# Kernel tuning notes

Hardware: AMD Instinct MI355X
Metric: run time of the kernel (lower is better)

## Reference

```python
import jax, jax.numpy as jnp
import numpy as np

B, C, H, E, K, QT = 256, 1024, 64, 64, 2, 20000

def _mlp(x, W1, b1, W2, b2):
    # GKT MLP (eval mode: dropout off; batch-norm omitted, see notes)
    return jax.nn.relu(jax.nn.relu(x @ W1 + b1) @ W2 + b2)

def setup_inputs() -> dict:
    key = jax.random.key(0)
    ks = jax.random.split(key, 30)
    s = 0.05  # weight scale to keep pre-clamp activations in a sane range
    xt = jax.random.uniform(ks[0], (B,), dtype=jnp.float32)
    qt = jax.random.randint(ks[1], (B,), 0, QT)
    ht = jax.random.normal(ks[2], (B, C, H), dtype=jnp.float32)
    # binary question->concept incidence, ~4 KCs per question, col 0 forced on
    oh = (jax.random.uniform(ks[3], (QT, C)) < 4.0 / C).astype(jnp.float32)
    oh = oh.at[:, 0].set(1.0)
    qt_kc_one_hot = jnp.concatenate([oh, jnp.zeros((1, C), jnp.float32)], axis=0)  # zero padding row
    kc_embeddings = jax.random.normal(ks[4], (C, E), dtype=jnp.float32) * 0.1
    graphs = jax.random.uniform(ks[5], (K, C, C), dtype=jnp.float32)  # graph_model output
    neigh_weight = jnp.float32(0.8)
    MI = H + E
    Ws1 = jax.random.normal(ks[6], (MI, H), jnp.float32) * s; bs1 = jnp.zeros((H,), jnp.float32)
    Ws2 = jax.random.normal(ks[7], (H, H), jnp.float32) * s;  bs2 = jnp.zeros((H,), jnp.float32)
    Wn1 = jax.random.normal(ks[8], (K, 2 * MI, H), jnp.float32) * s; bn1 = jnp.zeros((K, H), jnp.float32)
    Wn2 = jax.random.normal(ks[9], (K, H, H), jnp.float32) * s;      bn2 = jnp.zeros((K, H), jnp.float32)
    ea_w = jax.random.uniform(ks[10], (C,), dtype=jnp.float32)
    We = jax.random.normal(ks[11], (H, H), jnp.float32) * s; be = jnp.zeros((H,), jnp.float32)
    Wa = jax.random.normal(ks[12], (H, H), jnp.float32) * s; ba = jnp.zeros((H,), jnp.float32)
    W_ih = jax.random.normal(ks[13], (H, 3 * H), jnp.float32) * s; b_ih = jnp.zeros((3 * H,), jnp.float32)
    W_hh = jax.random.normal(ks[14], (H, 3 * H), jnp.float32) * s; b_hh = jnp.zeros((3 * H,), jnp.float32)
    Wp = jax.random.normal(ks[15], (H, 1), jnp.float32) * s; bp = jnp.zeros((1,), jnp.float32)
    return dict(xt=xt, qt=qt, ht=ht, qt_kc_one_hot=qt_kc_one_hot, kc_embeddings=kc_embeddings,
                graphs=graphs, neigh_weight=neigh_weight, Ws1=Ws1, bs1=bs1, Ws2=Ws2, bs2=bs2,
                Wn1=Wn1, bn1=bn1, Wn2=Wn2, bn2=bn2, ea_w=ea_w, We=We, be=be, Wa=Wa, ba=ba,
                W_ih=W_ih, b_ih=b_ih, W_hh=W_hh, b_hh=b_hh, Wp=Wp, bp=bp)

def reference(xt, qt, ht, qt_kc_one_hot, kc_embeddings, graphs, neigh_weight,
              Ws1, bs1, Ws2, bs2, Wn1, bn1, Wn2, bn2, ea_w, We, be, Wa, ba,
              W_ih, b_ih, W_hh, b_hh, Wp, bp):
    # ---- _aggregate: the fusion loops never write back, so tmp_ht = cat(ht, kc_emb)
    mask = qt_kc_one_hot[qt]                                   # [B, C] gather of binary incidence
    kc = jnp.broadcast_to(kc_embeddings[None], (mask.shape[0], C, E))
    tmp_ht = jnp.concatenate([ht, kc], axis=-1)                # [B, C, H+E]
    # ---- _agg_neighbors
    self_ht = tmp_ht * mask[..., None]
    self_feat = jnp.clip(_mlp(self_ht, Ws1, bs1, Ws2, bs2), -10.0, 10.0)
    neigh_ht = jnp.clip(jnp.concatenate([self_ht, tmp_ht], axis=-1), -5.0, 5.0)  # [B,C,2(H+E)]
    # bug-faithful adj: mean of graphs[k] rows over sample 0's active concepts
    a0 = mask[0]                                               # [C]
    denom = jnp.maximum(a0.sum(), 1.0)
    adj = jnp.clip(jnp.einsum('c,kcd->kd', a0, graphs) / denom, -5.0, 5.0)       # [K, C]
    nb = jax.vmap(lambda W1, b1, W2, b2: _mlp(neigh_ht, W1, b1, W2, b2))(Wn1, bn1, Wn2, bn2)
    nb = jnp.clip(nb, -5.0, 5.0)                               # [K, B, C, H]
    w = jnp.clip(neigh_weight, 0.1, 0.9)
    nf = jnp.clip(adj[0][None, :, None] * nb[0], -5.0, 5.0)
    for k in range(1, K):
        nf = jnp.clip(w * nf + (1.0 - w) * adj[k][None, :, None] * nb[k], -5.0, 5.0)
    m_next = jnp.clip(jnp.where(mask[..., None] > 0.5, self_feat, nf), -50.0, 50.0)
    # ---- erase-add gate
    g = ea_w[None, :, None]
    res = m_next - g * jax.nn.sigmoid(m_next @ We + be) * m_next + g * jnp.tanh(m_next @ Wa + ba)
    # ---- GRUCell over flattened (B*C) rows
    gi = res @ W_ih + b_ih
    gh = ht @ W_hh + b_hh
    ir, iz, in_ = jnp.split(gi, 3, axis=-1)
    hr, hz, hn = jnp.split(gh, 3, axis=-1)
    r = jax.nn.sigmoid(ir + hr)
    z = jax.nn.sigmoid(iz + hz)
    n = jnp.tanh(in_ + r * hn)
    h_next = (1.0 - z) * n + z * ht                            # [B, C, H]
    y = jax.nn.sigmoid(h_next @ Wp + bp)[..., 0]               # [B, C]
    return y
```

## Files before the change

### kernel.cpp

```cpp
#include <hip/hip_runtime.h>

#define DEVINL __device__ __forceinline__

typedef __bf16 bf16x8 __attribute__((ext_vector_type(8)));
typedef float  f32x4  __attribute__((ext_vector_type(4)));

static constexpr size_t kAdjOff  = 0;
static constexpr size_t kBiasOff = 8192;
static constexpr size_t kFragOff = 8192 + 786432;

static constexpr int FB_Wn1h0 = 0,  FB_Wn1h1 = 8,  FB_Wn2_0 = 16, FB_Wn2_1 = 24;
static constexpr int FB_Ws1h  = 32, FB_Ws2   = 40, FB_We    = 48, FB_Wa    = 56;
static constexpr int FB_Wih   = 64, FB_Whh   = 88;

DEVINL unsigned short bf16r(float f) {
  unsigned u = __builtin_bit_cast(unsigned, f);
  unsigned r = ((u >> 16) & 1u) + 0x7FFFu;
  return (unsigned short)((u + r) >> 16);
}
DEVINL float sigmoidf_(float x) { return __builtin_amdgcn_rcpf(1.f + __expf(-x)); }
DEVINL float tanhf_(float x)    { return 1.f - 2.f * __builtin_amdgcn_rcpf(1.f + __expf(2.f * x)); }

DEVINL void lds_fence() {
  __builtin_amdgcn_sched_barrier(0);
  __builtin_amdgcn_s_waitcnt(0xC07F);
  __builtin_amdgcn_sched_barrier(0);
}

DEVINL f32x4 mfma16(bf16x8 a, bf16x8 b, f32x4 c) {
  return __builtin_amdgcn_mfma_f32_16x16x32_bf16(a, b, c, 0, 0, 0);
}

DEVINL unsigned clip2_(unsigned x) {
  float lo = __builtin_bit_cast(float, x << 16);
  float hi = __builtin_bit_cast(float, x & 0xFFFF0000u);
  lo = fminf(fmaxf(lo, -5.f), 5.f);
  hi = fminf(fmaxf(hi, -5.f), 5.f);
  return (__builtin_bit_cast(unsigned, lo) >> 16) | (__builtin_bit_cast(unsigned, hi) & 0xFFFF0000u);
}
DEVINL bf16x8 clip5(bf16x8 a) {
  uint4 u = __builtin_bit_cast(uint4, a);
  u.x = clip2_(u.x); u.y = clip2_(u.y); u.z = clip2_(u.z); u.w = clip2_(u.w);
  return __builtin_bit_cast(bf16x8, u);
}

__global__ void prep_adj_kernel(const int* __restrict__ qt, const float* __restrict__ onehot,
                                const float* __restrict__ graphs, float* __restrict__ adjw) {
  __shared__ float a0v[1024];
  __shared__ int   aidx[1024];
  __shared__ int   s_nnz;
  __shared__ float s_den;
  const int tid = threadIdx.x;
  const int k = blockIdx.x >> 2, chunk = blockIdx.x & 3;
  if (tid == 0) { s_nnz = 0; s_den = 0.f; }
  __syncthreads();
  const int q0 = qt[0];
  float lsum = 0.f;
#pragma unroll
  for (int i = 0; i < 4; i++) {
    int c = tid * 4 + i;
    float v = onehot[(size_t)q0 * 1024 + c];
    lsum += v;
    if (v != 0.f) { int p = atomicAdd(&s_nnz, 1); aidx[p] = c; a0v[p] = v; }
  }
#pragma unroll
  for (int off = 32; off >= 1; off >>= 1) lsum += __shfl_xor(lsum, off, 64);
  if ((tid & 63) == 0) atomicAdd(&s_den, lsum);
  __syncthreads();
  const float denom = fmaxf(s_den, 1.f);
  const int nnz = s_nnz;
  const int d = chunk * 256 + tid;
  const float* G = graphs + (size_t)k * 1048576 + d;
  float sum = 0.f;
  for (int j = 0; j < nnz; j++) sum += a0v[j] * G[(size_t)aidx[j] * 1024];
  adjw[k * 1024 + d] = fminf(fmaxf(sum / denom, -5.f), 5.f);
}

__global__ void prep_bias_kernel(const float* __restrict__ kc, const float* __restrict__ Wn1,
                                 const float* __restrict__ bn1, const float* __restrict__ Ws1,
                                 const float* __restrict__ bs1, float* __restrict__ biasTab) {
  int gid = blockIdx.x * 256 + threadIdx.x;
  int j = gid & 63;
  int c = (gid >> 6) & 1023;
  int tab = gid >> 16;
  const float* kcr = kc + (size_t)c * 64;
  float s;
  if (tab < 2) {
    s = bn1[tab * 64 + j];
    const float* W = Wn1 + ((size_t)tab * 256 + 192) * 64 + j;
#pragma unroll 4
    for (int e = 0; e < 64; e++) s += fminf(fmaxf(kcr[e], -5.f), 5.f) * W[(size_t)e * 64];
  } else {
    s = bs1[j];
    const float* W = Ws1 + (size_t)64 * 64 + j;
#pragma unroll 4
    for (int e = 0; e < 64; e++) s += kcr[e] * W[(size_t)e * 64];
  }
  int c16 = c >> 4, rr = c & 3, qq = (c & 15) >> 2, nt = j >> 4;
  int lane = qq * 16 + (j & 15);
  biasTab[(size_t)((((c16 * 3 + tab) * 4 + nt) * 64 + lane)) * 4 + rr] = s;
}

__global__ void prep_wfrag_kernel(const float* __restrict__ Wn1, const float* __restrict__ Wn2,
                                  const float* __restrict__ Ws1, const float* __restrict__ Ws2,
                                  const float* __restrict__ We,  const float* __restrict__ Wa,
                                  const float* __restrict__ Wih, const float* __restrict__ Whh,
                                  uint4* __restrict__ wfrag) {
  const int bid = blockIdx.x, lane = threadIdx.x;
  int mat, ks, nt;
  if (bid < 64) { mat = bid >> 3; ks = (bid >> 2) & 1; nt = bid & 3; }
  else { int f2 = bid - 64; mat = 8 + f2 / 24; int f = f2 % 24; ks = f / 12; nt = f % 12; }
  const float* base = Wn1; int stride = 64;
  switch (mat) {
    case 0: base = Wn1 + (size_t)128 * 64; break;
    case 1: base = Wn1 + (size_t)(256 + 128) * 64; break;
    case 2: base = Wn2; break;
    case 3: base = Wn2 + (size_t)64 * 64; break;
    case 4: base = Ws1; break;
    case 5: base = Ws2; break;
    case 6: base = We; break;
    case 7: base = Wa; break;
    case 8: base = Wih; stride = 192; break;
    case 9: base = Whh; stride = 192; break;
  }
  const int qq = lane >> 4, col = nt * 16 + (lane & 15);
  union { unsigned short u[8]; uint4 v; } tmp;
#pragma unroll
  for (int jj = 0; jj < 8; jj++) {
    int k = ks * 32 + qq * 8 + jj;
    tmp.u[jj] = bf16r(base[(size_t)k * stride + col]);
  }
  wfrag[(size_t)bid * 64 + lane] = tmp.v;
}

__global__ __launch_bounds__(256, 2) void gkt_main_kernel(
    const int* __restrict__ qt, const float* __restrict__ onehot, const float* __restrict__ ht,
    const float* __restrict__ nw, const float* __restrict__ bn2, const float* __restrict__ be,
    const float* __restrict__ ba, const float* __restrict__ bih, const float* __restrict__ bhh,
    const float* __restrict__ Wp, const float* __restrict__ bp, const float* __restrict__ eaw,
    const float* __restrict__ bs2, const float* __restrict__ adjw, const float* __restrict__ biasTab,
    const bf16x8* __restrict__ wfrag, float* __restrict__ out) {
  __shared__ __align__(16) unsigned short hbuf[4][32][72];
  __shared__ __align__(16) float tokp[4][128];

  const int tid = threadIdx.x;
  const int wv = tid >> 6, lane = tid & 63;
  const int q = lane >> 4, cl = lane & 15;
  const int t0 = (blockIdx.x * 4 + wv) * 32;
  const int b = t0 >> 10, c0 = t0 & 1023, c16 = c0 >> 4;

  unsigned short* hb = &hbuf[wv][0][0];
  float* tp = &tokp[wv][0];

  if (lane < 32) {
    const int c = c0 + lane;
    tp[lane]      = onehot[(size_t)qt[b] * 1024 + c];
    tp[32 + lane] = adjw[c];
    tp[64 + lane] = adjw[1024 + c];
    tp[96 + lane] = eaw[c];
  }
  {
    const float4* ht4 = (const float4*)ht;
#pragma unroll
    for (int i = 0; i < 8; i++) {
      float4 v = ht4[(size_t)t0 * 16 + i * 64 + lane];
      int e = i * 64 + lane;
      int tok = e >> 4, coll = (e & 15) * 4;
      ushort4 h;
      h.x = bf16r(v.x); h.y = bf16r(v.y); h.z = bf16r(v.z); h.w = bf16r(v.w);
      *(ushort4*)&hbuf[wv][tok][coll] = h;
    }
  }
  lds_fence();

  const float wmix = fminf(fmaxf(nw[0], 0.1f), 0.9f);
  float wp4[4];
#pragma unroll
  for (int nt = 0; nt < 4; nt++) wp4[nt] = Wp[nt * 16 + cl];
  const float bpv = bp[0];

  auto ldA = [&](int mt, int ks) -> bf16x8 {
    return *(const bf16x8*)(hb + (cl + 16 * mt) * 72 + ks * 32 + q * 8);
  };
  auto ldB = [&](int frag) -> bf16x8 { return wfrag[frag * 64 + lane]; };
  auto ldTP4 = [&](int base, int mt) -> f32x4 {
    return *(const f32x4*)(tp + base + 16 * mt + q * 4);
  };
  const f32x4* bt4 = (const f32x4*)biasTab;

  bf16x8 xr[2][2];
#pragma unroll
  for (int mt = 0; mt < 2; mt++)
#pragma unroll
    for (int ks = 0; ks < 2; ks++) xr[mt][ks] = ldA(mt, ks);
  lds_fence();

  f32x4 nf[2][4];
  {
    bf16x8 xc[2][2];
#pragma unroll
    for (int mt = 0; mt < 2; mt++)
#pragma unroll
      for (int ks = 0; ks < 2; ks++) xc[mt][ks] = clip5(xr[mt][ks]);

#pragma unroll
    for (int k2 = 0; k2 < 2; k2++) {
      f32x4 acc[2][4];
#pragma unroll
      for (int mt = 0; mt < 2; mt++)
#pragma unroll
        for (int nt = 0; nt < 4; nt++)
          acc[mt][nt] = bt4[(((c16 + mt) * 3 + k2) * 4 + nt) * 64 + lane];
#pragma unroll
      for (int ks = 0; ks < 2; ks++)
#pragma unroll
        for (int nt = 0; nt < 4; nt++) {
          bf16x8 bb = ldB((k2 ? FB_Wn1h1 : FB_Wn1h0) + ks * 4 + nt);
          acc[0][nt] = mfma16(xc[0][ks], bb, acc[0][nt]);
          acc[1][nt] = mfma16(xc[1][ks], bb, acc[1][nt]);
        }
#pragma unroll
      for (int mt = 0; mt < 2; mt++)
#pragma unroll
        for (int nt = 0; nt < 4; nt++)
#pragma unroll
          for (int r = 0; r < 4; r++)
            hb[(16 * mt + q * 4 + r) * 72 + nt * 16 + cl] = bf16r(fmaxf(acc[mt][nt][r], 0.f));
      lds_fence();
      f32x4 acc2[2][4];
#pragma unroll
      for (int nt = 0; nt < 4; nt++) {
        float bz = bn2[k2 * 64 + nt * 16 + cl];
        f32x4 iv = {bz, bz, bz, bz};
        acc2[0][nt] = iv; acc2[1][nt] = iv;
      }
#pragma unroll
      for (int ks = 0; ks < 2; ks++) {
        bf16x8 a0 = ldA(0, ks), a1 = ldA(1, ks);
#pragma unroll
        for (int nt = 0; nt < 4; nt++) {
          bf16x8 bb = ldB((k2 ? FB_Wn2_1 : FB_Wn2_0) + ks * 4 + nt);
          acc2[0][nt] = mfma16(a0, bb, acc2[0][nt]);
          acc2[1][nt] = mfma16(a1, bb, acc2[1][nt]);
        }
      }
      lds_fence();
#pragma unroll
      for (int mt = 0; mt < 2; mt++) {
        f32x4 adjv = ldTP4((1 + k2) * 32, mt);
#pragma unroll
        for (int nt = 0; nt < 4; nt++)
#pragma unroll
          for (int r = 0; r < 4; r++) {
            float nb = fminf(fmaxf(acc2[mt][nt][r], 0.f), 5.f);
            float v = adjv[r] * nb;
            if (k2 == 0) nf[mt][nt][r] = wmix * fminf(fmaxf(v, -5.f), 5.f);
            else         nf[mt][nt][r] = fminf(fmaxf(nf[mt][nt][r] + (1.f - wmix) * v, -5.f), 5.f);
          }
      }
    }
  }

  bool anySelf = __any((lane < 32) && (tp[lane] > 0.5f));
  if (anySelf) {
    f32x4 acc[2][4];
#pragma unroll
    for (int mt = 0; mt < 2; mt++)
#pragma unroll
      for (int nt = 0; nt < 4; nt++)
        acc[mt][nt] = bt4[(((c16 + mt) * 3 + 2) * 4 + nt) * 64 + lane];
#pragma unroll
    for (int ks = 0; ks < 2; ks++)
#pragma unroll
      for (int nt = 0; nt < 4; nt++) {
        bf16x8 bb = ldB(FB_Ws1h + ks * 4 + nt);
        acc[0][nt] = mfma16(xr[0][ks], bb, acc[0][nt]);
        acc[1][nt] = mfma16(xr[1][ks], bb, acc[1][nt]);
      }
#pragma unroll
    for (int mt = 0; mt < 2; mt++)
#pragma unroll
      for (int nt = 0; nt < 4; nt++)
#pragma unroll
        for (int r = 0; r < 4; r++)
          hb[(16 * mt + q * 4 + r) * 72 + nt * 16 + cl] = bf16r(fmaxf(acc[mt][nt][r], 0.f));
    lds_fence();
    f32x4 acc2[2][4];
#pragma unroll
    for (int nt = 0; nt < 4; nt++) {
      float bz = bs2[nt * 16 + cl];
      f32x4 iv = {bz, bz, bz, bz};
      acc2[0][nt] = iv; acc2[1][nt] = iv;
    }
#pragma unroll
    for (int ks = 0; ks < 2; ks++) {
      bf16x8 a0 = ldA(0, ks), a1 = ldA(1, ks);
#pragma unroll
      for (int nt = 0; nt < 4; nt++) {
        bf16x8 bb = ldB(FB_Ws2 + ks * 4 + nt);
        acc2[0][nt] = mfma16(a0, bb, acc2[0][nt]);
        acc2[1][nt] = mfma16(a1, bb, acc2[1][nt]);
      }
    }
    lds_fence();
#pragma unroll
    for (int mt = 0; mt < 2; mt++) {
      f32x4 mk = ldTP4(0, mt);
#pragma unroll
      for (int nt = 0; nt < 4; nt++)
#pragma unroll
        for (int r = 0; r < 4; r++) {
          float sf = fminf(fmaxf(acc2[mt][nt][r], 0.f), 10.f);
          nf[mt][nt][r] = (mk[r] > 0.5f) ? sf : nf[mt][nt][r];
        }
    }
  }

#pragma unroll
  for (int mt = 0; mt < 2; mt++)
#pragma unroll
    for (int nt = 0; nt < 4; nt++)
#pragma unroll
      for (int r = 0; r < 4; r++)
        hb[(16 * mt + q * 4 + r) * 72 + nt * 16 + cl] = bf16r(nf[mt][nt][r]);
  lds_fence();
#pragma unroll
  for (int mt = 0; mt < 2; mt++) {
    bf16x8 mf0 = ldA(mt, 0), mf1 = ldA(mt, 1);
    f32x4 gv = ldTP4(96, mt);
    {
      f32x4 accE[4];
#pragma unroll
      for (int nt = 0; nt < 4; nt++) {
        float bz = be[nt * 16 + cl];
        accE[nt] = {bz, bz, bz, bz};
      }
#pragma unroll
      for (int nt = 0; nt < 4; nt++) {
        accE[nt] = mfma16(mf0, ldB(FB_We + nt), accE[nt]);
        accE[nt] = mfma16(mf1, ldB(FB_We + 4 + nt), accE[nt]);
      }
#pragma unroll
      for (int nt = 0; nt < 4; nt++)
#pragma unroll
        for (int r = 0; r < 4; r++) {
          float m = nf[mt][nt][r];
          nf[mt][nt][r] = m - gv[r] * sigmoidf_(accE[nt][r]) * m;
        }
    }
    {
      f32x4 accA[4];
#pragma unroll
      for (int nt = 0; nt < 4; nt++) {
        float bz = ba[nt * 16 + cl];
        accA[nt] = {bz, bz, bz, bz};
      }
#pragma unroll
      for (int nt = 0; nt < 4; nt++) {
        accA[nt] = mfma16(mf0, ldB(FB_Wa + nt), accA[nt]);
        accA[nt] = mfma16(mf1, ldB(FB_Wa + 4 + nt), accA[nt]);
      }
#pragma unroll
      for (int nt = 0; nt < 4; nt++)
#pragma unroll
        for (int r = 0; r < 4; r++)
          nf[mt][nt][r] += gv[r] * tanhf_(accA[nt][r]);
    }
  }

  lds_fence();
#pragma unroll
  for (int mt = 0; mt < 2; mt++)
#pragma unroll
    for (int nt = 0; nt < 4; nt++)
#pragma unroll
      for (int r = 0; r < 4; r++)
        hb[(16 * mt + q * 4 + r) * 72 + nt * 16 + cl] = bf16r(nf[mt][nt][r]);
  lds_fence();

#pragma unroll
  for (int mt = 0; mt < 2; mt++) {
    bf16x8 rf0 = ldA(mt, 0), rf1 = ldA(mt, 1);
    f32x4 gR[4], gZ[4], gN[4], gH[4];
#pragma unroll
    for (int nt = 0; nt < 4; nt++) {
      int col = nt * 16 + cl;
      float brz = bih[col] + bhh[col];
      float bzz = bih[64 + col] + bhh[64 + col];
      float bnn = bih[128 + col];
      float bhn = bhh[128 + col];
      gR[nt] = {brz, brz, brz, brz};
      gZ[nt] = {bzz, bzz, bzz, bzz};
      gN[nt] = {bnn, bnn, bnn, bnn};
      gH[nt] = {bhn, bhn, bhn, bhn};
    }
#pragma unroll
    for (int ks = 0; ks < 2; ks++) {
      bf16x8 rfk = ks ? rf1 : rf0;
      bf16x8 xrk = xr[mt][ks];
#pragma unroll
      for (int nt = 0; nt < 4; nt++) {
        gR[nt] = mfma16(rfk, ldB(FB_Wih + ks * 12 + nt), gR[nt]);
        gR[nt] = mfma16(xrk, ldB(FB_Whh + ks * 12 + nt), gR[nt]);
        gZ[nt] = mfma16(rfk, ldB(FB_Wih + ks * 12 + 4 + nt), gZ[nt]);
        gZ[nt] = mfma16(xrk, ldB(FB_Whh + ks * 12 + 4 + nt), gZ[nt]);
        gN[nt] = mfma16(rfk, ldB(FB_Wih + ks * 12 + 8 + nt), gN[nt]);
        gH[nt] = mfma16(xrk, ldB(FB_Whh + ks * 12 + 8 + nt), gH[nt]);
      }
    }
#pragma unroll
    for (int r = 0; r < 4; r++) {
      int tok = 16 * mt + q * 4 + r;
      float part = 0.f;
#pragma unroll
      for (int nt = 0; nt < 4; nt++) {
        float rr = sigmoidf_(gR[nt][r]);
        float zz = sigmoidf_(gZ[nt][r]);
        float nval = tanhf_(gN[nt][r] + rr * gH[nt][r]);
        float htv = ht[(size_t)(t0 + tok) * 64 + nt * 16 + cl];
        float hnx = (1.f - zz) * nval + zz * htv;
        part += hnx * wp4[nt];
      }
      part += __shfl_xor(part, 1, 64);
      part += __shfl_xor(part, 2, 64);
      part += __shfl_xor(part, 4, 64);
      part += __shfl_xor(part, 8, 64);
      if (cl == 0) out[t0 + tok] = sigmoidf_(part + bpv);
    }
  }
}

extern "C" void kernel_launch(void* const* d_in, const int* in_sizes, int n_in,
                              void* d_out, int out_size, void* d_ws, size_t ws_size,
                              hipStream_t stream) {
  const int*   qt     = (const int*)d_in[1];
  const float* ht     = (const float*)d_in[2];
  const float* onehot = (const float*)d_in[3];
  const float* kc     = (const float*)d_in[4];
  const float* graphs = (const float*)d_in[5];
  const float* nw     = (const float*)d_in[6];
  const float* Ws1    = (const float*)d_in[7];
  const float* bs1    = (const float*)d_in[8];
  const float* Ws2    = (const float*)d_in[9];
  const float* bs2    = (const float*)d_in[10];
  const float* Wn1    = (const float*)d_in[11];
  const float* bn1    = (const float*)d_in[12];
  const float* Wn2    = (const float*)d_in[13];
  const float* bn2    = (const float*)d_in[14];
  const float* eaw    = (const float*)d_in[15];
  const float* We     = (const float*)d_in[16];
  const float* be     = (const float*)d_in[17];
  const float* Wa     = (const float*)d_in[18];
  const float* ba     = (const float*)d_in[19];
  const float* Wih    = (const float*)d_in[20];
  const float* bih    = (const float*)d_in[21];
  const float* Whh    = (const float*)d_in[22];
  const float* bhh    = (const float*)d_in[23];
  const float* Wp     = (const float*)d_in[24];
  const float* bp     = (const float*)d_in[25];
  float* out = (float*)d_out;

  float* adjw    = (float*)((char*)d_ws + kAdjOff);
  float* biasTab = (float*)((char*)d_ws + kBiasOff);
  uint4* wfragU  = (uint4*)((char*)d_ws + kFragOff);

  prep_adj_kernel<<<8, 256, 0, stream>>>(qt, onehot, graphs, adjw);
  prep_bias_kernel<<<768, 256, 0, stream>>>(kc, Wn1, bn1, Ws1, bs1, biasTab);
  prep_wfrag_kernel<<<112, 64, 0, stream>>>(Wn1, Wn2, Ws1, Ws2, We, Wa, Wih, Whh, wfragU);
  gkt_main_kernel<<<2048, 256, 0, stream>>>(qt, onehot, ht, nw, bn2, be, ba, bih, bhh,
                                            Wp, bp, eaw, bs2, adjw, biasTab,
                                            (const bf16x8*)wfragU, out);
}
```

Baseline: 275.9 us.

## Transpose MFMA operands so accumulators hold token-major rows, vectorize LDS stores

Swaps the MFMA operand order so weights are the A operand and activations the B operand. Each lane's accumulator then holds 4 consecutive feature columns of one token, so bf16 results can be packed and written to LDS as 8-byte stores instead of scalar 2-byte stores. Biases, ht and Wp become float4 loads, the final dot-product reduction needs only two cross-lane shuffles, and the bias table layout is rearranged to match. The LDS scratch is widened to 136 columns so both Wn1 hidden halves and the pre- and post-gate activations live side by side, which removes some fences at the cost of more shared memory per block.

```diff
diff --git a/kernel.cpp b/kernel.cpp
--- a/kernel.cpp
+++ b/kernel.cpp
@@ -18,6 +18,13 @@
   unsigned r = ((u >> 16) & 1u) + 0x7FFFu;
   return (unsigned short)((u + r) >> 16);
 }
+DEVINL unsigned pack2(float a, float b) {
+  unsigned ua = __builtin_bit_cast(unsigned, a);
+  unsigned ub = __builtin_bit_cast(unsigned, b);
+  ua += ((ua >> 16) & 1u) + 0x7FFFu;
+  ub += ((ub >> 16) & 1u) + 0x7FFFu;
+  return (ua >> 16) | (ub & 0xFFFF0000u);
+}
 DEVINL float sigmoidf_(float x) { return __builtin_amdgcn_rcpf(1.f + __expf(-x)); }
 DEVINL float tanhf_(float x)    { return 1.f - 2.f * __builtin_amdgcn_rcpf(1.f + __expf(2.f * x)); }
 
@@ -27,8 +34,8 @@
   __builtin_amdgcn_sched_barrier(0);
 }
 
-DEVINL f32x4 mfma16(bf16x8 a, bf16x8 b, f32x4 c) {
-  return __builtin_amdgcn_mfma_f32_16x16x32_bf16(a, b, c, 0, 0, 0);
+DEVINL f32x4 mfmaWX(bf16x8 w, bf16x8 x, f32x4 c) {
+  return __builtin_amdgcn_mfma_f32_16x16x32_bf16(w, x, c, 0, 0, 0);
 }
 
 DEVINL unsigned clip2_(unsigned x) {
@@ -96,9 +103,8 @@
 #pragma unroll 4
     for (int e = 0; e < 64; e++) s += kcr[e] * W[(size_t)e * 64];
   }
-  int c16 = c >> 4, rr = c & 3, qq = (c & 15) >> 2, nt = j >> 4;
-  int lane = qq * 16 + (j & 15);
-  biasTab[(size_t)((((c16 * 3 + tab) * 4 + nt) * 64 + lane)) * 4 + rr] = s;
+  int c16p = c >> 4, cl2 = c & 15, nt = j >> 4, qq = (j >> 2) & 3, rr = j & 3;
+  biasTab[((size_t)(((c16p * 3 + tab) * 16 + cl2) * 4 + nt) * 4 + qq) * 4 + rr] = s;
 }
 
 __global__ void prep_wfrag_kernel(const float* __restrict__ Wn1, const float* __restrict__ Wn2,
@@ -140,7 +146,7 @@
     const float* __restrict__ Wp, const float* __restrict__ bp, const float* __restrict__ eaw,
     const float* __restrict__ bs2, const float* __restrict__ adjw, const float* __restrict__ biasTab,
     const bf16x8* __restrict__ wfrag, float* __restrict__ out) {
-  __shared__ __align__(16) unsigned short hbuf[4][32][72];
+  __shared__ __align__(16) unsigned short sbuf[4][32][136];
   __shared__ __align__(16) float tokp[4][128];
 
   const int tid = threadIdx.x;
@@ -149,7 +155,7 @@
   const int t0 = (blockIdx.x * 4 + wv) * 32;
   const int b = t0 >> 10, c0 = t0 & 1023, c16 = c0 >> 4;
 
-  unsigned short* hb = &hbuf[wv][0][0];
+  unsigned short* sb = &sbuf[wv][0][0];
   float* tp = &tokp[wv][0];
 
   if (lane < 32) {
@@ -166,33 +172,33 @@
       float4 v = ht4[(size_t)t0 * 16 + i * 64 + lane];
       int e = i * 64 + lane;
       int tok = e >> 4, coll = (e & 15) * 4;
-      ushort4 h;
-      h.x = bf16r(v.x); h.y = bf16r(v.y); h.z = bf16r(v.z); h.w = bf16r(v.w);
-      *(ushort4*)&hbuf[wv][tok][coll] = h;
+      uint2 p = {pack2(v.x, v.y), pack2(v.z, v.w)};
+      *(uint2*)&sbuf[wv][tok][coll] = p;
     }
   }
   lds_fence();
 
   const float wmix = fminf(fmaxf(nw[0], 0.1f), 0.9f);
-  float wp4[4];
-#pragma unroll
-  for (int nt = 0; nt < 4; nt++) wp4[nt] = Wp[nt * 16 + cl];
   const float bpv = bp[0];
 
-  auto ldA = [&](int mt, int ks) -> bf16x8 {
-    return *(const bf16x8*)(hb + (cl + 16 * mt) * 72 + ks * 32 + q * 8);
+  auto ldS = [&](int mt, int base) -> bf16x8 {
+    return *(const bf16x8*)(sb + (cl + 16 * mt) * 136 + base + q * 8);
   };
   auto ldB = [&](int frag) -> bf16x8 { return wfrag[frag * 64 + lane]; };
-  auto ldTP4 = [&](int base, int mt) -> f32x4 {
-    return *(const f32x4*)(tp + base + 16 * mt + q * 4);
+  auto stW = [&](int mt, int colb, f32x4 v) {
+    uint2 p = {pack2(v[0], v[1]), pack2(v[2], v[3])};
+    *(uint2*)(sb + (cl + 16 * mt) * 136 + colb) = p;
   };
   const f32x4* bt4 = (const f32x4*)biasTab;
+  auto ldBias = [&](int mt, int tab, int nt) -> f32x4 {
+    return bt4[(((c16 + mt) * 3 + tab) * 16 + cl) * 16 + nt * 4 + q];
+  };
 
   bf16x8 xr[2][2];
 #pragma unroll
   for (int mt = 0; mt < 2; mt++)
 #pragma unroll
-    for (int ks = 0; ks < 2; ks++) xr[mt][ks] = ldA(mt, ks);
+    for (int ks = 0; ks < 2; ks++) xr[mt][ks] = ldS(mt, ks * 32);
   lds_fence();
 
   f32x4 nf[2][4];
@@ -209,56 +215,60 @@
 #pragma unroll
       for (int mt = 0; mt < 2; mt++)
 #pragma unroll
-        for (int nt = 0; nt < 4; nt++)
-          acc[mt][nt] = bt4[(((c16 + mt) * 3 + k2) * 4 + nt) * 64 + lane];
+        for (int nt = 0; nt < 4; nt++) acc[mt][nt] = ldBias(mt, k2, nt);
 #pragma unroll
       for (int ks = 0; ks < 2; ks++)
 #pragma unroll
         for (int nt = 0; nt < 4; nt++) {
           bf16x8 bb = ldB((k2 ? FB_Wn1h1 : FB_Wn1h0) + ks * 4 + nt);
-          acc[0][nt] = mfma16(xc[0][ks], bb, acc[0][nt]);
-          acc[1][nt] = mfma16(xc[1][ks], bb, acc[1][nt]);
+          acc[0][nt] = mfmaWX(bb, xc[0][ks], acc[0][nt]);
+          acc[1][nt] = mfmaWX(bb, xc[1][ks], acc[1][nt]);
         }
 #pragma unroll
       for (int mt = 0; mt < 2; mt++)
 #pragma unroll
-        for (int nt = 0; nt < 4; nt++)
-#pragma unroll
-          for (int r = 0; r < 4; r++)
-            hb[(16 * mt + q * 4 + r) * 72 + nt * 16 + cl] = bf16r(fmaxf(acc[mt][nt][r], 0.f));
-      lds_fence();
+        for (int nt = 0; nt < 4; nt++) {
+          f32x4 rv;
+#pragma unroll
+          for (int r = 0; r < 4; r++) rv[r] = fmaxf(acc[mt][nt][r], 0.f);
+          stW(mt, k2 * 64 + nt * 16 + q * 4, rv);
+        }
+    }
+    lds_fence();
+
+#pragma unroll
+    for (int k2 = 0; k2 < 2; k2++) {
       f32x4 acc2[2][4];
 #pragma unroll
       for (int nt = 0; nt < 4; nt++) {
-        float bz = bn2[k2 * 64 + nt * 16 + cl];
-        f32x4 iv = {bz, bz, bz, bz};
-        acc2[0][nt] = iv; acc2[1][nt] = iv;
+        f32x4 bz = *(const f32x4*)(bn2 + k2 * 64 + nt * 16 + q * 4);
+        acc2[0][nt] = bz; acc2[1][nt] = bz;
       }
 #pragma unroll
       for (int ks = 0; ks < 2; ks++) {
-        bf16x8 a0 = ldA(0, ks), a1 = ldA(1, ks);
+        bf16x8 a0 = ldS(0, k2 * 64 + ks * 32), a1 = ldS(1, k2 * 64 + ks * 32);
 #pragma unroll
         for (int nt = 0; nt < 4; nt++) {
           bf16x8 bb = ldB((k2 ? FB_Wn2_1 : FB_Wn2_0) + ks * 4 + nt);
-          acc2[0][nt] = mfma16(a0, bb, acc2[0][nt]);
-          acc2[1][nt] = mfma16(a1, bb, acc2[1][nt]);
+          acc2[0][nt] = mfmaWX(bb, a0, acc2[0][nt]);
+          acc2[1][nt] = mfmaWX(bb, a1, acc2[1][nt]);
         }
       }
-      lds_fence();
 #pragma unroll
       for (int mt = 0; mt < 2; mt++) {
-        f32x4 adjv = ldTP4((1 + k2) * 32, mt);
+        float adjv = tp[(1 + k2) * 32 + 16 * mt + cl];
 #pragma unroll
         for (int nt = 0; nt < 4; nt++)
 #pragma unroll
           for (int r = 0; r < 4; r++) {
             float nb = fminf(fmaxf(acc2[mt][nt][r], 0.f), 5.f);
-            float v = adjv[r] * nb;
+            float v = adjv * nb;
             if (k2 == 0) nf[mt][nt][r] = wmix * fminf(fmaxf(v, -5.f), 5.f);
             else         nf[mt][nt][r] = fminf(fmaxf(nf[mt][nt][r] + (1.f - wmix) * v, -5.f), 5.f);
           }
       }
     }
+    lds_fence();
   }
 
   bool anySelf = __any((lane < 32) && (tp[lane] > 0.5f));
@@ -267,51 +277,51 @@
 #pragma unroll
     for (int mt = 0; mt < 2; mt++)
 #pragma unroll
-      for (int nt = 0; nt < 4; nt++)
-        acc[mt][nt] = bt4[(((c16 + mt) * 3 + 2) * 4 + nt) * 64 + lane];
+      for (int nt = 0; nt < 4; nt++) acc[mt][nt] = ldBias(mt, 2, nt);
 #pragma unroll
     for (int ks = 0; ks < 2; ks++)
 #pragma unroll
       for (int nt = 0; nt < 4; nt++) {
         bf16x8 bb = ldB(FB_Ws1h + ks * 4 + nt);
-        acc[0][nt] = mfma16(xr[0][ks], bb, acc[0][nt]);
-        acc[1][nt] = mfma16(xr[1][ks], bb, acc[1][nt]);
+        acc[0][nt] = mfmaWX(bb, xr[0][ks], acc[0][nt]);
+        acc[1][nt] = mfmaWX(bb, xr[1][ks], acc[1][nt]);
       }
 #pragma unroll
     for (int mt = 0; mt < 2; mt++)
 #pragma unroll
-      for (int nt = 0; nt < 4; nt++)
-#pragma unroll
-        for (int r = 0; r < 4; r++)
-          hb[(16 * mt + q * 4 + r) * 72 + nt * 16 + cl] = bf16r(fmaxf(acc[mt][nt][r], 0.f));
+      for (int nt = 0; nt < 4; nt++) {
+        f32x4 rv;
+#pragma unroll
+        for (int r = 0; r < 4; r++) rv[r] = fmaxf(acc[mt][nt][r], 0.f);
+        stW(mt, nt * 16 + q * 4, rv);
+      }
     lds_fence();
     f32x4 acc2[2][4];
 #pragma unroll
     for (int nt = 0; nt < 4; nt++) {
-      float bz = bs2[nt * 16 + cl];
-      f32x4 iv = {bz, bz, bz, bz};
-      acc2[0][nt] = iv; acc2[1][nt] = iv;
+      f32x4 bz = *(const f32x4*)(bs2 + nt * 16 + q * 4);
+      acc2[0][nt] = bz; acc2[1][nt] = bz;
     }
 #pragma unroll
     for (int ks = 0; ks < 2; ks++) {
-      bf16x8 a0 = ldA(0, ks), a1 = ldA(1, ks);
+      bf16x8 a0 = ldS(0, ks * 32), a1 = ldS(1, ks * 32);
 #pragma unroll
       for (int nt = 0; nt < 4; nt++) {
         bf16x8 bb = ldB(FB_Ws2 + ks * 4 + nt);
-        acc2[0][nt] = mfma16(a0, bb, acc2[0][nt]);
-        acc2[1][nt] = mfma16(a1, bb, acc2[1][nt]);
+        acc2[0][nt] = mfmaWX(bb, a0, acc2[0][nt]);
+        acc2[1][nt] = mfmaWX(bb, a1, acc2[1][nt]);
       }
     }
     lds_fence();
 #pragma unroll
     for (int mt = 0; mt < 2; mt++) {
-      f32x4 mk = ldTP4(0, mt);
+      float mk = tp[16 * mt + cl];
 #pragma unroll
       for (int nt = 0; nt < 4; nt++)
 #pragma unroll
         for (int r = 0; r < 4; r++) {
           float sf = fminf(fmaxf(acc2[mt][nt][r], 0.f), 10.f);
-          nf[mt][nt][r] = (mk[r] > 0.5f) ? sf : nf[mt][nt][r];
+          nf[mt][nt][r] = (mk > 0.5f) ? sf : nf[mt][nt][r];
         }
     }
   }
@@ -319,80 +329,60 @@
 #pragma unroll
   for (int mt = 0; mt < 2; mt++)
 #pragma unroll
+    for (int nt = 0; nt < 4; nt++) stW(mt, nt * 16 + q * 4, nf[mt][nt]);
+  lds_fence();
+
+#pragma unroll
+  for (int mt = 0; mt < 2; mt++) {
+    bf16x8 mf0 = ldS(mt, 0), mf1 = ldS(mt, 32);
+    float gvs = tp[96 + 16 * mt + cl];
+    f32x4 accE[4];
+#pragma unroll
+    for (int nt = 0; nt < 4; nt++) accE[nt] = *(const f32x4*)(be + nt * 16 + q * 4);
+#pragma unroll
+    for (int nt = 0; nt < 4; nt++) {
+      accE[nt] = mfmaWX(ldB(FB_We + nt), mf0, accE[nt]);
+      accE[nt] = mfmaWX(ldB(FB_We + 4 + nt), mf1, accE[nt]);
+    }
+#pragma unroll
     for (int nt = 0; nt < 4; nt++)
 #pragma unroll
+      for (int r = 0; r < 4; r++) {
+        float m = nf[mt][nt][r];
+        nf[mt][nt][r] = m - gvs * sigmoidf_(accE[nt][r]) * m;
+      }
+    f32x4 accA[4];
+#pragma unroll
+    for (int nt = 0; nt < 4; nt++) accA[nt] = *(const f32x4*)(ba + nt * 16 + q * 4);
+#pragma unroll
+    for (int nt = 0; nt < 4; nt++) {
+      accA[nt] = mfmaWX(ldB(FB_Wa + nt), mf0, accA[nt]);
+      accA[nt] = mfmaWX(ldB(FB_Wa + 4 + nt), mf1, accA[nt]);
+    }
+#pragma unroll
+    for (int nt = 0; nt < 4; nt++)
+#pragma unroll
       for (int r = 0; r < 4; r++)
-        hb[(16 * mt + q * 4 + r) * 72 + nt * 16 + cl] = bf16r(nf[mt][nt][r]);
+        nf[mt][nt][r] += gvs * tanhf_(accA[nt][r]);
+  }
+
+#pragma unroll
+  for (int mt = 0; mt < 2; mt++)
+#pragma unroll
+    for (int nt = 0; nt < 4; nt++) stW(mt, 64 + nt * 16 + q * 4, nf[mt][nt]);
   lds_fence();
+
 #pragma unroll
   for (int mt = 0; mt < 2; mt++) {
-    bf16x8 mf0 = ldA(mt, 0), mf1 = ldA(mt, 1);
-    f32x4 gv = ldTP4(96, mt);
-    {
-      f32x4 accE[4];
-#pragma unroll
-      for (int nt = 0; nt < 4; nt++) {
-        float bz = be[nt * 16 + cl];
-        accE[nt] = {bz, bz, bz, bz};
-      }
-#pragma unroll
-      for (int nt = 0; nt < 4; nt++) {
-        accE[nt] = mfma16(mf0, ldB(FB_We + nt), accE[nt]);
-        accE[nt] = mfma16(mf1, ldB(FB_We + 4 + nt), accE[nt]);
-      }
-#pragma unroll
-      for (int nt = 0; nt < 4; nt++)
-#pragma unroll
-        for (int r = 0; r < 4; r++) {
-          float m = nf[mt][nt][r];
-          nf[mt][nt][r] = m - gv[r] * sigmoidf_(accE[nt][r]) * m;
-        }
-    }
-    {
-      f32x4 accA[4];
-#pragma unroll
-      for (int nt = 0; nt < 4; nt++) {
-        float bz = ba[nt * 16 + cl];
-        accA[nt] = {bz, bz, bz, bz};
-      }
-#pragma unroll
-      for (int nt = 0; nt < 4; nt++) {
-        accA[nt] = mfma16(mf0, ldB(FB_Wa + nt), accA[nt]);
-        accA[nt] = mfma16(mf1, ldB(FB_Wa + 4 + nt), accA[nt]);
-      }
-#pragma unroll
-      for (int nt = 0; nt < 4; nt++)
-#pragma unroll
-        for (int r = 0; r < 4; r++)
-          nf[mt][nt][r] += gv[r] * tanhf_(accA[nt][r]);
-    }
-  }
-
-  lds_fence();
-#pragma unroll
-  for (int mt = 0; mt < 2; mt++)
-#pragma unroll
-    for (int nt = 0; nt < 4; nt++)
-#pragma unroll
-      for (int r = 0; r < 4; r++)
-        hb[(16 * mt + q * 4 + r) * 72 + nt * 16 + cl] = bf16r(nf[mt][nt][r]);
-  lds_fence();
-
-#pragma unroll
-  for (int mt = 0; mt < 2; mt++) {
-    bf16x8 rf0 = ldA(mt, 0), rf1 = ldA(mt, 1);
-    f32x4 gR[4], gZ[4], gN[4], gH[4];
+    bf16x8 rf0 = ldS(mt, 64), rf1 = ldS(mt, 96);
+    f32x4 gRv[4], gZv[4], gNv[4], gHv[4];
 #pragma unroll
     for (int nt = 0; nt < 4; nt++) {
-      int col = nt * 16 + cl;
-      float brz = bih[col] + bhh[col];
-      float bzz = bih[64 + col] + bhh[64 + col];
-      float bnn = bih[128 + col];
-      float bhn = bhh[128 + col];
-      gR[nt] = {brz, brz, brz, brz};
-      gZ[nt] = {bzz, bzz, bzz, bzz};
-      gN[nt] = {bnn, bnn, bnn, bnn};
-      gH[nt] = {bhn, bhn, bhn, bhn};
+      int j0 = nt * 16 + q * 4;
+      gRv[nt] = *(const f32x4*)(bih + j0)       + *(const f32x4*)(bhh + j0);
+      gZv[nt] = *(const f32x4*)(bih + 64 + j0)  + *(const f32x4*)(bhh + 64 + j0);
+      gNv[nt] = *(const f32x4*)(bih + 128 + j0);
+      gHv[nt] = *(const f32x4*)(bhh + 128 + j0);
     }
 #pragma unroll
     for (int ks = 0; ks < 2; ks++) {
@@ -400,33 +390,31 @@
       bf16x8 xrk = xr[mt][ks];
 #pragma unroll
       for (int nt = 0; nt < 4; nt++) {
-        gR[nt] = mfma16(rfk, ldB(FB_Wih + ks * 12 + nt), gR[nt]);
-        gR[nt] = mfma16(xrk, ldB(FB_Whh + ks * 12 + nt), gR[nt]);
-        gZ[nt] = mfma16(rfk, ldB(FB_Wih + ks * 12 + 4 + nt), gZ[nt]);
-        gZ[nt] = mfma16(xrk, ldB(FB_Whh + ks * 12 + 4 + nt), gZ[nt]);
-        gN[nt] = mfma16(rfk, ldB(FB_Wih + ks * 12 + 8 + nt), gN[nt]);
-        gH[nt] = mfma16(xrk, ldB(FB_Whh + ks * 12 + 8 + nt), gH[nt]);
-      }
-    }
-#pragma unroll
-    for (int r = 0; r < 4; r++) {
-      int tok = 16 * mt + q * 4 + r;
-      float part = 0.f;
-#pragma unroll
-      for (int nt = 0; nt < 4; nt++) {
-        float rr = sigmoidf_(gR[nt][r]);
-        float zz = sigmoidf_(gZ[nt][r]);
-        float nval = tanhf_(gN[nt][r] + rr * gH[nt][r]);
-        float htv = ht[(size_t)(t0 + tok) * 64 + nt * 16 + cl];
-        float hnx = (1.f - zz) * nval + zz * htv;
-        part += hnx * wp4[nt];
-      }
-      part += __shfl_xor(part, 1, 64);
-      part += __shfl_xor(part, 2, 64);
-      part += __shfl_xor(part, 4, 64);
-      part += __shfl_xor(part, 8, 64);
-      if (cl == 0) out[t0 + tok] = sigmoidf_(part + bpv);
-    }
+        gRv[nt] = mfmaWX(ldB(FB_Wih + ks * 12 + nt), rfk, gRv[nt]);
+        gRv[nt] = mfmaWX(ldB(FB_Whh + ks * 12 + nt), xrk, gRv[nt]);
+        gZv[nt] = mfmaWX(ldB(FB_Wih + ks * 12 + 4 + nt), rfk, gZv[nt]);
+        gZv[nt] = mfmaWX(ldB(FB_Whh + ks * 12 + 4 + nt), xrk, gZv[nt]);
+        gNv[nt] = mfmaWX(ldB(FB_Wih + ks * 12 + 8 + nt), rfk, gNv[nt]);
+        gHv[nt] = mfmaWX(ldB(FB_Whh + ks * 12 + 8 + nt), xrk, gHv[nt]);
+      }
+    }
+    float part = 0.f;
+#pragma unroll
+    for (int nt = 0; nt < 4; nt++) {
+      f32x4 wpv = *(const f32x4*)(Wp + nt * 16 + q * 4);
+      f32x4 htv = *(const f32x4*)(ht + (size_t)(t0 + 16 * mt + cl) * 64 + nt * 16 + q * 4);
+#pragma unroll
+      for (int r = 0; r < 4; r++) {
+        float rr = sigmoidf_(gRv[nt][r]);
+        float zz = sigmoidf_(gZv[nt][r]);
+        float nv = tanhf_(gNv[nt][r] + rr * gHv[nt][r]);
+        float hnx = (1.f - zz) * nv + zz * htv[r];
+        part += hnx * wpv[r];
+      }
+    }
+    part += __shfl_xor(part, 16, 64);
+    part += __shfl_xor(part, 32, 64);
+    if (lane < 16) out[t0 + 16 * mt + lane] = sigmoidf_(part + bpv);
   }
 }
 
```

Result: slower. 293.0 us (+6.2%).
